# Kernel optimization log

Hardware: AMD Instinct MI355X
Metric: run time of the kernel (lower is better)

Reference implementation:

```python
import math
import jax, jax.numpy as jnp
import numpy as np

B, N, HID, NH = 4, 1024, 1024, 16
DH = HID // NH
MLP = int(HID * 4.0)


def _ndense(x, w):
    # NormalizedDense: row-normalize kernel (axis=1 for 2D), alpha=sqrt(w[0].size)=sqrt(out),
    # then divide by sqrt(fan_in).
    norm = jnp.linalg.norm(w, axis=1, keepdims=True)
    alpha = jnp.sqrt(jnp.asarray(w.shape[1], x.dtype))
    wn = w / (norm * alpha + 1e-4)
    wn = wn / jnp.sqrt(jnp.asarray(w.shape[0], x.dtype))
    return x @ wn


def mp_silu(x):
    return jax.nn.silu(x) / 0.596


def pixel_norm(x, eps=1e-4):
    return x * jax.lax.rsqrt(jnp.mean(x * x, axis=-1, keepdims=True) + eps)


def mp_add(a, b, t=0.3):
    return ((1 - t) * a + t * b) / math.sqrt((1 - t) ** 2 + t ** 2)


def setup_inputs() -> dict:
    key = jax.random.key(0)
    ks = jax.random.split(key, 9)
    std = 0.02
    return {
        "x": jax.random.normal(ks[0], (B, N, HID), jnp.float32),
        "c": jax.random.normal(ks[1], (B, HID), jnp.float32),
        "w_cond": std * jax.random.normal(ks[2], (HID, 2 * HID), jnp.float32),
        "w_qkv": std * jax.random.normal(ks[3], (HID, 3 * HID), jnp.float32),
        "w_out": std * jax.random.normal(ks[4], (HID, HID), jnp.float32),
        "w_mlp1": std * jax.random.normal(ks[5], (HID, MLP), jnp.float32),
        "w_mlp2": std * jax.random.normal(ks[6], (MLP, HID), jnp.float32),
        "attn_gain": 0.1 * jax.random.normal(ks[7], (), jnp.float32),
        "mlp_gain": 0.1 * jax.random.normal(ks[8], (), jnp.float32),
    }


def reference(x, c, w_cond, w_qkv, w_out, w_mlp1, w_mlp2, attn_gain, mlp_gain):
    # conditioning -> gain/shift
    cc = mp_silu(c)
    cc = _ndense(cc, w_cond)                       # [B, 2H]
    gain, shift = jnp.split(cc, 2, axis=-1)        # [B, H] each

    # attention branch
    x_cond = pixel_norm(x) * (1 + gain[:, None]) + shift[:, None]
    qkv = _ndense(x_cond, w_qkv)                   # [B, N, 3H]
    q, k, v = jnp.split(qkv, 3, axis=-1)
    q, k, v = pixel_norm(q), pixel_norm(k), pixel_norm(v)

    def split_heads(t):
        return t.reshape(B, N, NH, DH).transpose(0, 2, 1, 3)  # [B, NH, N, DH]

    q, k, v = split_heads(q), split_heads(k), split_heads(v)
    q = q / jnp.sqrt(jnp.sum(q * q, axis=-1, keepdims=True) + 1e-6)
    k = k / jnp.sqrt(jnp.sum(k * k, axis=-1, keepdims=True) + 1e-6)

    attn = jnp.einsum('bhnd,bhmd->bhnm', q, k) / math.sqrt(DH)
    attn = jax.nn.softmax(attn, axis=-1)
    x_attn = jnp.einsum('bhnm,bhmd->bhnd', attn, v)
    x_attn = x_attn.transpose(0, 2, 1, 3).reshape(B, N, HID)
    x_attn = pixel_norm(_ndense(x_attn, w_out)) * jnp.exp(attn_gain)
    x = mp_add(x, x_attn, t=0.3)

    # MLP branch
    x_cond = pixel_norm(x) * (1 + gain[:, None]) + shift[:, None]
    h = mp_silu(pixel_norm(_ndense(x_cond, w_mlp1)))
    x_mlp = pixel_norm(_ndense(h, w_mlp2)) * jnp.exp(mlp_gain)
    x = mp_add(x, x_mlp, t=0.3)
    return x
```

## Files before the change

kernel.cpp:

```cpp
#include <hip/hip_runtime.h>

typedef __bf16 bf16_t;
typedef __attribute__((ext_vector_type(8))) __bf16 bh8;
typedef __attribute__((ext_vector_type(4))) __bf16 bh4;
typedef __attribute__((ext_vector_type(4))) float f32x4;

#define DEV static __device__ __forceinline__

typedef __attribute__((address_space(3))) void lds_void;
typedef const __attribute__((address_space(1))) void glb_void;

DEV void async16(const bf16_t* g, bf16_t* l) {
  __builtin_amdgcn_global_load_lds((glb_void*)g, (lds_void*)l, 16, 0, 0);
}

#define GBAR() asm volatile("s_barrier" ::: "memory")
#define VMW(n) asm volatile("s_waitcnt vmcnt(" #n ")" ::: "memory")

DEV f32x4 mfma16(bh8 a, bh8 b, f32x4 c) {
  return __builtin_amdgcn_mfma_f32_16x16x32_bf16(a, b, c, 0, 0, 0);
}

DEV float wave_sum(float v) {
#pragma unroll
  for (int m = 32; m > 0; m >>= 1) v += __shfl_xor(v, m, 64);
  return v;
}

DEV float block_sum(float v, float* sbuf) {
  v = wave_sum(v);
  int wid = threadIdx.x >> 6;
  if ((threadIdx.x & 63) == 0) sbuf[wid] = v;
  __syncthreads();
  float r = sbuf[0] + sbuf[1] + sbuf[2] + sbuf[3];
  __syncthreads();
  return r;
}

__global__ void k_wnorm_all(const float* __restrict__ w_cond, const float* __restrict__ w_qkv,
                            const float* __restrict__ w_out, const float* __restrict__ w_mlp1,
                            const float* __restrict__ w_mlp2, float* __restrict__ s) {
  __shared__ float sbuf[4];
  int id = blockIdx.x;
  const float* W; int N, K, row;
  if (id < 1024)      { W = w_cond; N = 2048; K = 1024; row = id; }
  else if (id < 2048) { W = w_qkv;  N = 3072; K = 1024; row = id - 1024; }
  else if (id < 3072) { W = w_out;  N = 1024; K = 1024; row = id - 2048; }
  else if (id < 4096) { W = w_mlp1; N = 4096; K = 1024; row = id - 3072; }
  else                { W = w_mlp2; N = 1024; K = 4096; row = id - 4096; }
  const float4* wr = (const float4*)(W + (size_t)row * N);
  float acc = 0.f;
  for (int i = threadIdx.x; i < (N >> 2); i += 256) {
    float4 w = wr[i];
    acc += w.x*w.x + w.y*w.y + w.z*w.z + w.w*w.w;
  }
  float tot = block_sum(acc, sbuf);
  if (threadIdx.x == 0) {
    float norm = sqrtf(tot);
    s[id] = 1.0f / ((norm * sqrtf((float)N) + 1e-4f) * sqrtf((float)K));
  }
}

__global__ void k_wtrans_all(const float* __restrict__ w_cond, const float* __restrict__ w_qkv,
                             const float* __restrict__ w_out, const float* __restrict__ w_mlp1,
                             const float* __restrict__ w_mlp2, const float* __restrict__ sall,
                             bf16_t* __restrict__ wt_cond, bf16_t* __restrict__ wt_qkv,
                             bf16_t* __restrict__ wt_out, bf16_t* __restrict__ wt_mlp1,
                             bf16_t* __restrict__ wt_mlp2) {
  __shared__ float tile[64][65];
  int id = blockIdx.x;
  const float* W; const float* s; bf16_t* Wt; int K, N, n0, k0;
  if (id < 512)       { W=w_cond; s=sall;      Wt=wt_cond; K=1024; N=2048; int l=id;      n0=(l&31)*64; k0=(l>>5)*64; }
  else if (id < 1280) { W=w_qkv;  s=sall+1024; Wt=wt_qkv;  K=1024; N=3072; int l=id-512;  n0=(l%48)*64; k0=(l/48)*64; }
  else if (id < 1536) { W=w_out;  s=sall+2048; Wt=wt_out;  K=1024; N=1024; int l=id-1280; n0=(l&15)*64; k0=(l>>4)*64; }
  else if (id < 2560) { W=w_mlp1; s=sall+3072; Wt=wt_mlp1; K=1024; N=4096; int l=id-1536; n0=(l&63)*64; k0=(l>>6)*64; }
  else                { W=w_mlp2; s=sall+4096; Wt=wt_mlp2; K=4096; N=1024; int l=id-2560; n0=(l&15)*64; k0=(l>>4)*64; }
  int tx = threadIdx.x & 63, ty = threadIdx.x >> 6;
  for (int r = ty; r < 64; r += 4)
    tile[r][tx] = W[(size_t)(k0 + r) * N + n0 + tx] * s[k0 + r];
  __syncthreads();
  for (int r = ty; r < 64; r += 4)
    Wt[(size_t)(n0 + r) * K + k0 + tx] = (bf16_t)tile[tx][r];
}

__global__ void k_cond(const float* __restrict__ c, const bf16_t* __restrict__ wt,
                       float* __restrict__ gs) {
  __shared__ float cc[4][1024];
  int t = threadIdx.x;
  for (int i = t; i < 4096; i += 256) {
    int b = i >> 10, col = i & 1023;
    float x = c[b * 1024 + col];
    float sig = 1.f / (1.f + __expf(-x));
    cc[b][col] = x * sig * (1.f / 0.596f);
  }
  __syncthreads();
  int wid = t >> 6, lane = t & 63;
  int j = blockIdx.x * 4 + wid;
  const bf16_t* wr = wt + (size_t)j * 1024;
  float acc0 = 0, acc1 = 0, acc2 = 0, acc3 = 0;
  for (int i = lane; i < 1024; i += 64) {
    float w = (float)wr[i];
    acc0 += cc[0][i] * w; acc1 += cc[1][i] * w;
    acc2 += cc[2][i] * w; acc3 += cc[3][i] * w;
  }
  float v0 = wave_sum(acc0), v1 = wave_sum(acc1), v2 = wave_sum(acc2), v3 = wave_sum(acc3);
  if (lane == 0) {
    gs[0 * 2048 + j] = v0; gs[1 * 2048 + j] = v1;
    gs[2 * 2048 + j] = v2; gs[3 * 2048 + j] = v3;
  }
}

__global__ void k_xcond(const float* __restrict__ x, const float* __restrict__ gs,
                        bf16_t* __restrict__ xc) {
  __shared__ float sbuf[4];
  int row = blockIdx.x, b = row >> 10, t = threadIdx.x;
  float4 v = ((const float4*)(x + (size_t)row * 1024))[t];
  float ss = v.x*v.x + v.y*v.y + v.z*v.z + v.w*v.w;
  float tot = block_sum(ss, sbuf);
  float r = rsqrtf(tot * (1.f/1024.f) + 1e-4f);
  float4 g  = ((const float4*)(gs + b * 2048))[t];
  float4 sh = ((const float4*)(gs + b * 2048 + 1024))[t];
  bh4 o;
  o[0] = (bf16_t)(v.x * r * (1.f + g.x) + sh.x);
  o[1] = (bf16_t)(v.y * r * (1.f + g.y) + sh.y);
  o[2] = (bf16_t)(v.z * r * (1.f + g.z) + sh.z);
  o[3] = (bf16_t)(v.w * r * (1.f + g.w) + sh.w);
  *(bh4*)(xc + (size_t)row * 1024 + t * 4) = o;
}

__global__ __launch_bounds__(512, 2) void k_gemm8(const bf16_t* __restrict__ A,
                                                  const bf16_t* __restrict__ Bt,
                                                  bf16_t* __restrict__ C,
                                                  int M, int N, int K, int klen) {
  __shared__ __attribute__((aligned(16))) bf16_t As[2][2][256][32];
  __shared__ __attribute__((aligned(16))) bf16_t Bs[2][2][256][32];
  const int ntn = gridDim.x;
  const unsigned flat = blockIdx.x + ntn * blockIdx.y;
  const unsigned q = (ntn * gridDim.y) >> 3;
  const unsigned wg = (flat & 7) * q + (flat >> 3);
  const int m0 = (int)(wg / (unsigned)ntn) * 256;
  const int n0 = (int)(wg % (unsigned)ntn) * 256;
  const size_t kbeg = (size_t)blockIdx.z * klen;
  C += (size_t)blockIdx.z * M * N;
  const int t = threadIdx.x, lane = t & 63;
  const int wm = (t >> 6) >> 2, wn = (t >> 6) & 3;
  const int l15 = lane & 15, quad = lane >> 4;
  const int q8 = (quad ^ ((l15 >> 2) & 2)) * 8;
  const int rA = wm * 128 + l15;
  const int rB = wn * 64 + l15;
  const int sr = t >> 2;
  const int sc = ((t & 3) << 3) ^ ((t & 32) >> 1);
  const int swv = (t >> 6) * 512;
  const bf16_t* AgS = A + (size_t)(m0 + sr) * K + kbeg + sc;
  const bf16_t* BgS = Bt + (size_t)(n0 + sr) * K + kbeg + sc;
  const size_t rstep = (size_t)128 * K;
  const int NT = klen >> 6;
  f32x4 acc[8][4] = {};

#define STG_A(kt_, h_, bb_) { const bf16_t* g = AgS + (kt_) * 64 + (h_) * 32; \
    bf16_t* l = &As[bb_][h_][0][0] + swv; async16(g, l); async16(g + rstep, l + 4096); }
#define STG_B(kt_, h_, bb_) { const bf16_t* g = BgS + (kt_) * 64 + (h_) * 32; \
    bf16_t* l = &Bs[bb_][h_][0][0] + swv; async16(g, l); async16(g + rstep, l + 4096); }

  STG_B(0, 0, 0); STG_B(0, 1, 0);
  STG_A(0, 0, 0); STG_A(0, 1, 0);
  if (NT > 1) { STG_B(1, 0, 1); STG_B(1, 1, 1); VMW(4); } else { VMW(0); }
  GBAR();

  for (int kt = 0; kt < NT; ++kt) {
    const int bb = kt & 1;
    bh8 a[4][2], b[4][2];
#pragma unroll
    for (int m = 0; m < 4; ++m)
#pragma unroll
      for (int kc = 0; kc < 2; ++kc)
        a[m][kc] = *(const bh8*)&As[bb][kc][rA + m * 16][q8];
#pragma unroll
    for (int n = 0; n < 2; ++n)
#pragma unroll
      for (int kc = 0; kc < 2; ++kc)
        b[n][kc] = *(const bh8*)&Bs[bb][kc][rB + n * 16][q8];
    if (kt + 1 < NT) STG_A(kt + 1, 0, bb ^ 1);
    GBAR();
    __builtin_amdgcn_s_setprio(1);
#pragma unroll
    for (int m = 0; m < 4; ++m)
#pragma unroll
      for (int n = 0; n < 2; ++n)
#pragma unroll
        for (int kc = 0; kc < 2; ++kc)
          acc[m][n] = mfma16(a[m][kc], b[n][kc], acc[m][n]);
    __builtin_amdgcn_s_setprio(0);
    GBAR();
#pragma unroll
    for (int n = 0; n < 2; ++n)
#pragma unroll
      for (int kc = 0; kc < 2; ++kc)
        b[2 + n][kc] = *(const bh8*)&Bs[bb][kc][rB + (2 + n) * 16][q8];
    if (kt + 1 < NT) STG_A(kt + 1, 1, bb ^ 1);
    GBAR();
    __builtin_amdgcn_s_setprio(1);
#pragma unroll
    for (int m = 0; m < 4; ++m)
#pragma unroll
      for (int n = 0; n < 2; ++n)
#pragma unroll
        for (int kc = 0; kc < 2; ++kc)
          acc[m][2 + n] = mfma16(a[m][kc], b[2 + n][kc], acc[m][2 + n]);
    __builtin_amdgcn_s_setprio(0);
    GBAR();
#pragma unroll
    for (int m = 0; m < 4; ++m)
#pragma unroll
      for (int kc = 0; kc < 2; ++kc)
        a[m][kc] = *(const bh8*)&As[bb][kc][rA + 64 + m * 16][q8];
    if (kt + 2 < NT) STG_B(kt + 2, 0, bb);
    GBAR();
    __builtin_amdgcn_s_setprio(1);
#pragma unroll
    for (int m = 0; m < 4; ++m)
#pragma unroll
      for (int n = 0; n < 2; ++n)
#pragma unroll
        for (int kc = 0; kc < 2; ++kc)
          acc[4 + m][n] = mfma16(a[m][kc], b[n][kc], acc[4 + m][n]);
    __builtin_amdgcn_s_setprio(0);
    GBAR();
    if (kt + 2 < NT) STG_B(kt + 2, 1, bb);
    __builtin_amdgcn_s_setprio(1);
#pragma unroll
    for (int m = 0; m < 4; ++m)
#pragma unroll
      for (int n = 0; n < 2; ++n)
#pragma unroll
        for (int kc = 0; kc < 2; ++kc)
          acc[4 + m][2 + n] = mfma16(a[m][kc], b[2 + n][kc], acc[4 + m][2 + n]);
    __builtin_amdgcn_s_setprio(0);
    if (kt + 2 < NT) { VMW(4); } else { VMW(0); }
    GBAR();
  }
#undef STG_A
#undef STG_B

  const int cm = m0 + wm * 128 + quad * 4;
  const int cn = n0 + wn * 64 + l15;
#pragma unroll
  for (int m = 0; m < 8; ++m)
#pragma unroll
    for (int n = 0; n < 4; ++n)
#pragma unroll
      for (int r2 = 0; r2 < 4; ++r2)
        C[(size_t)(cm + m * 16 + r2) * N + cn + n * 16] = (bf16_t)acc[m][n][r2];
}

__global__ void k_qkvnorm(const bf16_t* __restrict__ qkv, bf16_t* __restrict__ qo,
                          bf16_t* __restrict__ ko, bf16_t* __restrict__ vo) {
  __shared__ float sbuf[4];
  const int row = blockIdx.x, b = row >> 10, n = row & 1023, t = threadIdx.x;
  const bf16_t* rp = qkv + (size_t)row * 3072;
  bh4 q4 = *(const bh4*)(rp + t * 4);
  bh4 k4 = *(const bh4*)(rp + 1024 + t * 4);
  bh4 v4 = *(const bh4*)(rp + 2048 + t * 4);
  float4 q = {(float)q4[0], (float)q4[1], (float)q4[2], (float)q4[3]};
  float4 k = {(float)k4[0], (float)k4[1], (float)k4[2], (float)k4[3]};
  float4 v = {(float)v4[0], (float)v4[1], (float)v4[2], (float)v4[3]};
  float sq = q.x*q.x + q.y*q.y + q.z*q.z + q.w*q.w;
  float sk = k.x*k.x + k.y*k.y + k.z*k.z + k.w*k.w;
  float sv = v.x*v.x + v.y*v.y + v.z*v.z + v.w*v.w;
  float tq = block_sum(sq, sbuf);
  float tk = block_sum(sk, sbuf);
  float tv = block_sum(sv, sbuf);
  float rq = rsqrtf(tq * (1.f/1024.f) + 1e-4f);
  float rk = rsqrtf(tk * (1.f/1024.f) + 1e-4f);
  float rv = rsqrtf(tv * (1.f/1024.f) + 1e-4f);
  float hq = sq, hk = sk;
#pragma unroll
  for (int m = 1; m < 16; m <<= 1) { hq += __shfl_xor(hq, m, 64); hk += __shfl_xor(hk, m, 64); }
  float qs = rq * rsqrtf(rq*rq*hq + 1e-6f);
  float ks = rk * rsqrtf(rk*rk*hk + 1e-6f);
  int h = t >> 4, d = (t & 15) * 4;
  size_t base = ((size_t)(b * 16 + h) * 1024 + n) * 64 + d;
  bh4 oq, okk, ov;
  oq[0]=(bf16_t)(q.x*qs); oq[1]=(bf16_t)(q.y*qs); oq[2]=(bf16_t)(q.z*qs); oq[3]=(bf16_t)(q.w*qs);
  okk[0]=(bf16_t)(k.x*ks); okk[1]=(bf16_t)(k.y*ks); okk[2]=(bf16_t)(k.z*ks); okk[3]=(bf16_t)(k.w*ks);
  ov[0]=(bf16_t)(v.x*rv); ov[1]=(bf16_t)(v.y*rv); ov[2]=(bf16_t)(v.z*rv); ov[3]=(bf16_t)(v.w*rv);
  *(bh4*)(qo + base) = oq;
  *(bh4*)(ko + base) = okk;
  *(bh4*)(vo + base) = ov;
}

__global__ void k_vtrans(const bf16_t* __restrict__ vh, bf16_t* __restrict__ vt) {
  __shared__ bf16_t tile[64][72];
  const int n0 = blockIdx.x * 64, bh = blockIdx.y;
  const int t = threadIdx.x;
  const bf16_t* src = vh + ((size_t)bh * 1024 + n0) * 64;
#pragma unroll
  for (int i = t; i < 512; i += 256) {
    int r = i >> 3, p = (i & 7) * 8;
    *(bh8*)&tile[r][p] = *(const bh8*)(src + r * 64 + p);
  }
  __syncthreads();
  bf16_t* dst = vt + (size_t)bh * 64 * 1024 + n0;
#pragma unroll
  for (int i = t; i < 512; i += 256) {
    int d = i & 63, nch = (i >> 6) * 8;
    bh8 o;
#pragma unroll
    for (int j = 0; j < 8; j++) o[j] = tile[nch + j][d];
    *(bh8*)(dst + (size_t)d * 1024 + nch) = o;
  }
}

__global__ __launch_bounds__(256) void k_attn(const bf16_t* __restrict__ Q,
                                              const bf16_t* __restrict__ K,
                                              const bf16_t* __restrict__ Vt_g,
                                              bf16_t* __restrict__ O) {
  __shared__ bf16_t Qs[64][72];
  __shared__ bf16_t Ks[64][72];
  __shared__ bf16_t Vt[64][72];
  __shared__ bf16_t Ps[64][72];
  const int qt = blockIdx.x, bh = blockIdx.y;
  const int b = bh >> 4, h = bh & 15;
  const int t = threadIdx.x, lane = t & 63, wid = t >> 6;
  const int l15 = lane & 15, quad = lane >> 4;
  const int strip = wid * 16;
  const bf16_t* Qg = Q + ((size_t)bh * 1024 + qt * 64) * 64;
  const bf16_t* Kg = K + (size_t)bh * 1024 * 64;
  const bf16_t* Vg = Vt_g + (size_t)bh * 64 * 1024;
  for (int i = t; i < 512; i += 256) {
    int r = i >> 3, p = (i & 7) * 8;
    *(bh8*)&Qs[r][p] = *(const bh8*)(Qg + r * 64 + p);
  }
  f32x4 o[4] = {};
  float rs[4] = {};
  __syncthreads();
  for (int kv0 = 0; kv0 < 1024; kv0 += 64) {
    for (int i = t; i < 512; i += 256) {
      int r = i >> 3, p = (i & 7) * 8;
      *(bh8*)&Ks[r][p] = *(const bh8*)(Kg + (size_t)(kv0 + r) * 64 + p);
      *(bh8*)&Vt[r][p] = *(const bh8*)(Vg + (size_t)r * 1024 + kv0 + p);
    }
    __syncthreads();
    f32x4 s[4] = {};
#pragma unroll
    for (int kc = 0; kc < 2; kc++) {
      bh8 aq = *(const bh8*)&Qs[strip + l15][kc*32 + quad*8];
      bh8 bk[4];
#pragma unroll
      for (int j = 0; j < 4; j++) bk[j] = *(const bh8*)&Ks[j*16 + l15][kc*32 + quad*8];
#pragma unroll
      for (int j = 0; j < 4; j++)
        s[j] = __builtin_amdgcn_mfma_f32_16x16x32_bf16(aq, bk[j], s[j], 0, 0, 0);
    }
#pragma unroll
    for (int j = 0; j < 4; j++)
#pragma unroll
      for (int r = 0; r < 4; r++) {
        float p = __expf(s[j][r] * 0.125f);
        bf16_t pb = (bf16_t)p;
        rs[r] += (float)pb;
        Ps[strip + quad*4 + r][j*16 + l15] = pb;
      }
#pragma unroll
    for (int kc = 0; kc < 2; kc++) {
      bh8 ap = *(const bh8*)&Ps[strip + l15][kc*32 + quad*8];
      bh8 bv[4];
#pragma unroll
      for (int j = 0; j < 4; j++) bv[j] = *(const bh8*)&Vt[j*16 + l15][kc*32 + quad*8];
#pragma unroll
      for (int j = 0; j < 4; j++)
        o[j] = __builtin_amdgcn_mfma_f32_16x16x32_bf16(ap, bv[j], o[j], 0, 0, 0);
    }
    __syncthreads();
  }
#pragma unroll
  for (int r = 0; r < 4; r++) {
    float v = rs[r];
    v += __shfl_xor(v, 1, 64); v += __shfl_xor(v, 2, 64);
    v += __shfl_xor(v, 4, 64); v += __shfl_xor(v, 8, 64);
    float inv = 1.f / v;
    int n = qt * 64 + strip + quad*4 + r;
#pragma unroll
    for (int j = 0; j < 4; j++)
      O[((size_t)b * 1024 + n) * 1024 + h*64 + j*16 + l15] = (bf16_t)(o[j][r] * inv);
  }
}

__global__ void k_amerge(const bf16_t* __restrict__ y, const float* __restrict__ x,
                         const float* __restrict__ gs, const float* __restrict__ again,
                         bf16_t* __restrict__ x1, bf16_t* __restrict__ xc2) {
  __shared__ float sbuf[4];
  int row = blockIdx.x, b = row >> 10, t = threadIdx.x;
  const size_t PS = (size_t)4096 * 1024;
  float4 yv = {0.f, 0.f, 0.f, 0.f};
#pragma unroll
  for (int p = 0; p < 4; p++) {
    bh4 a = *(const bh4*)(y + p * PS + (size_t)row * 1024 + t * 4);
    yv.x += (float)a[0]; yv.y += (float)a[1]; yv.z += (float)a[2]; yv.w += (float)a[3];
  }
  float4 xv = ((const float4*)(x + (size_t)row * 1024))[t];
  float ss = yv.x*yv.x + yv.y*yv.y + yv.z*yv.z + yv.w*yv.w;
  float tot = block_sum(ss, sbuf);
  float r = rsqrtf(tot * (1.f/1024.f) + 1e-4f);
  float ag = __expf(again[0]);
  const float C1 = 0.7f / 0.76157731059f, C2 = 0.3f / 0.76157731059f;
  float4 xo;
  xo.x = C1 * xv.x + C2 * (yv.x * r * ag);
  xo.y = C1 * xv.y + C2 * (yv.y * r * ag);
  xo.z = C1 * xv.z + C2 * (yv.z * r * ag);
  xo.w = C1 * xv.w + C2 * (yv.w * r * ag);
  bh4 x1o;
  x1o[0] = (bf16_t)xo.x; x1o[1] = (bf16_t)xo.y; x1o[2] = (bf16_t)xo.z; x1o[3] = (bf16_t)xo.w;
  *(bh4*)(x1 + (size_t)row * 1024 + t * 4) = x1o;
  float ss1 = xo.x*xo.x + xo.y*xo.y + xo.z*xo.z + xo.w*xo.w;
  float tot1 = block_sum(ss1, sbuf);
  float r1 = rsqrtf(tot1 * (1.f/1024.f) + 1e-4f);
  float4 g  = ((const float4*)(gs + b * 2048))[t];
  float4 sh = ((const float4*)(gs + b * 2048 + 1024))[t];
  bh4 o;
  o[0] = (bf16_t)(xo.x * r1 * (1.f + g.x) + sh.x);
  o[1] = (bf16_t)(xo.y * r1 * (1.f + g.y) + sh.y);
  o[2] = (bf16_t)(xo.z * r1 * (1.f + g.z) + sh.z);
  o[3] = (bf16_t)(xo.w * r1 * (1.f + g.w) + sh.w);
  *(bh4*)(xc2 + (size_t)row * 1024 + t * 4) = o;
}

__global__ void k_mlpnorm(const bf16_t* __restrict__ hf, bf16_t* __restrict__ hb) {
  __shared__ float sbuf[4];
  int row = blockIdx.x, t = threadIdx.x;
  const bf16_t* rp = hf + (size_t)row * 4096;
  float4 v[4]; float ss = 0.f;
#pragma unroll
  for (int i = 0; i < 4; i++) {
    bh4 bv = *(const bh4*)(rp + (t + 256 * i) * 4);
    v[i].x = (float)bv[0]; v[i].y = (float)bv[1]; v[i].z = (float)bv[2]; v[i].w = (float)bv[3];
    ss += v[i].x*v[i].x + v[i].y*v[i].y + v[i].z*v[i].z + v[i].w*v[i].w;
  }
  float tot = block_sum(ss, sbuf);
  float r = rsqrtf(tot * (1.f/4096.f) + 1e-4f);
#pragma unroll
  for (int i = 0; i < 4; i++) {
    float a[4] = {v[i].x, v[i].y, v[i].z, v[i].w};
    bh4 o;
#pragma unroll
    for (int j = 0; j < 4; j++) {
      float u = a[j] * r;
      float sig = 1.f / (1.f + __expf(-u));
      o[j] = (bf16_t)(u * sig * (1.f / 0.596f));
    }
    *(bh4*)(hb + (size_t)row * 4096 + (t + 256 * i) * 4) = o;
  }
}

__global__ void k_fmerge(const bf16_t* __restrict__ y, const bf16_t* __restrict__ x1,
                         const float* __restrict__ mgain, float* __restrict__ out) {
  __shared__ float sbuf[4];
  int row = blockIdx.x, t = threadIdx.x;
  const size_t PS = (size_t)4096 * 1024;
  float4 yv = {0.f, 0.f, 0.f, 0.f};
#pragma unroll
  for (int p = 0; p < 4; p++) {
    bh4 yp = *(const bh4*)(y + p * PS + (size_t)row * 1024 + t * 4);
    yv.x += (float)yp[0]; yv.y += (float)yp[1]; yv.z += (float)yp[2]; yv.w += (float)yp[3];
  }
  bh4 xb = *(const bh4*)(x1 + (size_t)row * 1024 + t * 4);
  float4 xv = {(float)xb[0], (float)xb[1], (float)xb[2], (float)xb[3]};
  float ss = yv.x*yv.x + yv.y*yv.y + yv.z*yv.z + yv.w*yv.w;
  float tot = block_sum(ss, sbuf);
  float r = rsqrtf(tot * (1.f/1024.f) + 1e-4f);
  float mg = __expf(mgain[0]);
  const float C1 = 0.7f / 0.76157731059f, C2 = 0.3f / 0.76157731059f;
  float4 o;
  o.x = C1 * xv.x + C2 * (yv.x * r * mg);
  o.y = C1 * xv.y + C2 * (yv.y * r * mg);
  o.z = C1 * xv.z + C2 * (yv.z * r * mg);
  o.w = C1 * xv.w + C2 * (yv.w * r * mg);
  ((float4*)(out + (size_t)row * 1024))[t] = o;
}

extern "C" void kernel_launch(void* const* d_in, const int* in_sizes, int n_in,
                              void* d_out, int out_size, void* d_ws, size_t ws_size,
                              hipStream_t stream) {
  const float* x      = (const float*)d_in[0];
  const float* c      = (const float*)d_in[1];
  const float* w_cond = (const float*)d_in[2];
  const float* w_qkv  = (const float*)d_in[3];
  const float* w_out  = (const float*)d_in[4];
  const float* w_mlp1 = (const float*)d_in[5];
  const float* w_mlp2 = (const float*)d_in[6];
  const float* again  = (const float*)d_in[7];
  const float* mgain  = (const float*)d_in[8];
  float* out = (float*)d_out;
  char* ws = (char*)d_ws;

  bf16_t* wt_cond = (bf16_t*)(ws + 0);
  bf16_t* wt_qkv  = (bf16_t*)(ws + 4194304);
  bf16_t* wt_out  = (bf16_t*)(ws + 10485760);
  bf16_t* wt_mlp1 = (bf16_t*)(ws + 12582912);
  bf16_t* wt_mlp2 = (bf16_t*)(ws + 20971520);
  float*  sn      = (float*)(ws + 29360128);
  float*  gs      = (float*)(ws + 29392896);
  bf16_t* xc      = (bf16_t*)(ws + 29425664);
  bf16_t* qh      = (bf16_t*)(ws + 37814272);
  bf16_t* kh      = (bf16_t*)(ws + 46202880);
  bf16_t* vh      = (bf16_t*)(ws + 54591488);
  bf16_t* xattn   = (bf16_t*)(ws + 62980096);
  bf16_t* hb      = (bf16_t*)(ws + 37814272);
  bf16_t* x1      = (bf16_t*)(ws + 71368704);
  bf16_t* vt      = (bf16_t*)(ws + 79757312);
  bf16_t* buf_b   = (bf16_t*)(ws + 88145920);

  k_wnorm_all<<<8192, 256, 0, stream>>>(w_cond, w_qkv, w_out, w_mlp1, w_mlp2, sn);
  k_wtrans_all<<<3584, 256, 0, stream>>>(w_cond, w_qkv, w_out, w_mlp1, w_mlp2, sn,
                                         wt_cond, wt_qkv, wt_out, wt_mlp1, wt_mlp2);

  k_cond<<<512, 256, 0, stream>>>(c, wt_cond, gs);
  k_xcond<<<4096, 256, 0, stream>>>(x, gs, xc);
  k_gemm8<<<dim3(12, 16, 1), 512, 0, stream>>>(xc, wt_qkv, buf_b, 4096, 3072, 1024, 1024);
  k_qkvnorm<<<4096, 256, 0, stream>>>(buf_b, qh, kh, vh);
  k_vtrans<<<dim3(16, 64), 256, 0, stream>>>(vh, vt);
  k_attn<<<dim3(16, 64), 256, 0, stream>>>(qh, kh, vt, xattn);
  k_gemm8<<<dim3(4, 16, 4), 512, 0, stream>>>(xattn, wt_out, buf_b, 4096, 1024, 1024, 256);
  k_amerge<<<4096, 256, 0, stream>>>(buf_b, x, gs, again, x1, xc);
  k_gemm8<<<dim3(16, 16, 1), 512, 0, stream>>>(xc, wt_mlp1, buf_b, 4096, 4096, 1024, 1024);
  k_mlpnorm<<<4096, 256, 0, stream>>>(buf_b, hb);
  k_gemm8<<<dim3(4, 16, 4), 512, 0, stream>>>(hb, wt_mlp2, buf_b, 4096, 1024, 4096, 1024);
  k_fmerge<<<4096, 256, 0, stream>>>(buf_b, x1, mgain, out);
  (void)in_sizes; (void)n_in; (void)out_size; (void)ws_size;
}
```

Baseline: 368.9 us.

## Restructure attention kernel with async double-buffered K/V, swizzled LDS, 128-row Q tiles

Rewrites the attention kernel so each block handles 128 query rows (two 16-row fragments per wave) and streams K/V tiles with async global-to-LDS loads into double buffers, overlapping the next tile's load with the current tile's compute. LDS tiles drop their padding and use XOR swizzling to avoid bank conflicts. Grid blocks are remapped so neighbouring blocks share heads, and MFMA sections are wrapped in s_setprio. The aim is to hide memory latency and reuse each K/V tile across twice as many queries. The cost is more registers per thread and fewer blocks in the grid.

```diff
diff --git a/kernel.cpp b/kernel.cpp
--- a/kernel.cpp
+++ b/kernel.cpp
@@ -19,6 +19,14 @@
 
 DEV f32x4 mfma16(bh8 a, bh8 b, f32x4 c) {
   return __builtin_amdgcn_mfma_f32_16x16x32_bf16(a, b, c, 0, 0, 0);
+}
+
+DEV const bf16_t* lds7(const bf16_t* base, int row, int c) {
+  return base + row * 64 + ((c ^ (row & 7)) << 3);
+}
+DEV bf16_t* ldsP(bf16_t* base, int row, int c) {
+  int m = (row & 7) ^ ((row >> 3) & 1);
+  return base + row * 64 + ((c ^ m) << 3);
 }
 
 DEV float wave_sum(float v) {
@@ -311,79 +319,121 @@
   }
 }
 
-__global__ __launch_bounds__(256) void k_attn(const bf16_t* __restrict__ Q,
-                                              const bf16_t* __restrict__ K,
-                                              const bf16_t* __restrict__ Vt_g,
-                                              bf16_t* __restrict__ O) {
-  __shared__ bf16_t Qs[64][72];
-  __shared__ bf16_t Ks[64][72];
-  __shared__ bf16_t Vt[64][72];
-  __shared__ bf16_t Ps[64][72];
-  const int qt = blockIdx.x, bh = blockIdx.y;
+__global__ __launch_bounds__(256, 2) void k_attn(const bf16_t* __restrict__ Q,
+                                                 const bf16_t* __restrict__ K,
+                                                 const bf16_t* __restrict__ Vt_g,
+                                                 bf16_t* __restrict__ O) {
+  __shared__ __attribute__((aligned(16))) bf16_t Qs[128][64];
+  __shared__ __attribute__((aligned(16))) bf16_t Ks[2][64][64];
+  __shared__ __attribute__((aligned(16))) bf16_t Vt[2][64][64];
+  __shared__ __attribute__((aligned(16))) bf16_t Ps[128][64];
+  const unsigned flat = blockIdx.x + 8u * blockIdx.y;
+  const int qt = (int)((flat >> 3) & 7);
+  const int bh = (int)((flat & 7) * 8 + (flat >> 6));
   const int b = bh >> 4, h = bh & 15;
   const int t = threadIdx.x, lane = t & 63, wid = t >> 6;
   const int l15 = lane & 15, quad = lane >> 4;
-  const int strip = wid * 16;
-  const bf16_t* Qg = Q + ((size_t)bh * 1024 + qt * 64) * 64;
+  const int strip = wid * 32;
+  const int srow = t >> 3;
+  const int scol = ((t & 7) ^ (srow & 7)) << 3;
+  const int swv = wid * 512;
+  const bf16_t* Qg = Q + ((size_t)bh * 1024 + qt * 128) * 64;
   const bf16_t* Kg = K + (size_t)bh * 1024 * 64;
   const bf16_t* Vg = Vt_g + (size_t)bh * 64 * 1024;
-  for (int i = t; i < 512; i += 256) {
-    int r = i >> 3, p = (i & 7) * 8;
-    *(bh8*)&Qs[r][p] = *(const bh8*)(Qg + r * 64 + p);
-  }
-  f32x4 o[4] = {};
-  float rs[4] = {};
-  __syncthreads();
-  for (int kv0 = 0; kv0 < 1024; kv0 += 64) {
-    for (int i = t; i < 512; i += 256) {
-      int r = i >> 3, p = (i & 7) * 8;
-      *(bh8*)&Ks[r][p] = *(const bh8*)(Kg + (size_t)(kv0 + r) * 64 + p);
-      *(bh8*)&Vt[r][p] = *(const bh8*)(Vg + (size_t)r * 1024 + kv0 + p);
+
+#pragma unroll
+  for (int c2 = 0; c2 < 4; ++c2)
+    async16(Qg + (size_t)(c2 * 32 + srow) * 64 + scol, &Qs[0][0] + c2 * 2048 + swv);
+#pragma unroll
+  for (int r0 = 0; r0 < 64; r0 += 32) {
+    async16(Kg + (size_t)(r0 + srow) * 64 + scol, &Ks[0][0][0] + r0 * 64 + swv);
+    async16(Vg + (size_t)(r0 + srow) * 1024 + scol, &Vt[0][0][0] + r0 * 64 + swv);
+  }
+  VMW(0);
+  GBAR();
+
+  f32x4 o[2][4] = {};
+  float rs[2][4] = {{}, {}};
+  for (int kt = 0; kt < 16; ++kt) {
+    const int bb = kt & 1;
+    const int kv0 = kt * 64;
+    if (kt < 15) {
+#pragma unroll
+      for (int r0 = 0; r0 < 64; r0 += 32) {
+        async16(Kg + (size_t)(kv0 + 64 + r0 + srow) * 64 + scol,
+                &Ks[bb ^ 1][0][0] + r0 * 64 + swv);
+        async16(Vg + (size_t)(r0 + srow) * 1024 + kv0 + 64 + scol,
+                &Vt[bb ^ 1][0][0] + r0 * 64 + swv);
+      }
     }
-    __syncthreads();
-    f32x4 s[4] = {};
-#pragma unroll
-    for (int kc = 0; kc < 2; kc++) {
-      bh8 aq = *(const bh8*)&Qs[strip + l15][kc*32 + quad*8];
-      bh8 bk[4];
-#pragma unroll
-      for (int j = 0; j < 4; j++) bk[j] = *(const bh8*)&Ks[j*16 + l15][kc*32 + quad*8];
-#pragma unroll
-      for (int j = 0; j < 4; j++)
-        s[j] = __builtin_amdgcn_mfma_f32_16x16x32_bf16(aq, bk[j], s[j], 0, 0, 0);
+    f32x4 s[2][4] = {};
+    bh8 aq[2][2], bk[4][2];
+#pragma unroll
+    for (int rf = 0; rf < 2; ++rf)
+#pragma unroll
+      for (int kc = 0; kc < 2; ++kc)
+        aq[rf][kc] = *(const bh8*)lds7(&Qs[0][0], strip + rf * 16 + l15, kc * 4 + quad);
+#pragma unroll
+    for (int j = 0; j < 4; ++j)
+#pragma unroll
+      for (int kc = 0; kc < 2; ++kc)
+        bk[j][kc] = *(const bh8*)lds7(&Ks[bb][0][0], j * 16 + l15, kc * 4 + quad);
+    __builtin_amdgcn_s_setprio(1);
+#pragma unroll
+    for (int rf = 0; rf < 2; ++rf)
+#pragma unroll
+      for (int j = 0; j < 4; ++j)
+#pragma unroll
+        for (int kc = 0; kc < 2; ++kc)
+          s[rf][j] = mfma16(aq[rf][kc], bk[j][kc], s[rf][j]);
+    __builtin_amdgcn_s_setprio(0);
+#pragma unroll
+    for (int rf = 0; rf < 2; ++rf)
+#pragma unroll
+      for (int j = 0; j < 4; ++j)
+#pragma unroll
+        for (int r = 0; r < 4; ++r) {
+          float p = __expf(s[rf][j][r] * 0.125f);
+          bf16_t pb = (bf16_t)p;
+          rs[rf][r] += (float)pb;
+          int prow = strip + rf * 16 + quad * 4 + r;
+          ldsP(&Ps[0][0], prow, j * 2 + (l15 >> 3))[l15 & 7] = pb;
+        }
+    bh8 ap[2][2], bv[4][2];
+#pragma unroll
+    for (int rf = 0; rf < 2; ++rf)
+#pragma unroll
+      for (int kc = 0; kc < 2; ++kc)
+        ap[rf][kc] = *(const bh8*)ldsP(&Ps[0][0], strip + rf * 16 + l15, kc * 4 + quad);
+#pragma unroll
+    for (int j = 0; j < 4; ++j)
+#pragma unroll
+      for (int kc = 0; kc < 2; ++kc)
+        bv[j][kc] = *(const bh8*)lds7(&Vt[bb][0][0], j * 16 + l15, kc * 4 + quad);
+    __builtin_amdgcn_s_setprio(1);
+#pragma unroll
+    for (int rf = 0; rf < 2; ++rf)
+#pragma unroll
+      for (int j = 0; j < 4; ++j)
+#pragma unroll
+        for (int kc = 0; kc < 2; ++kc)
+          o[rf][j] = mfma16(ap[rf][kc], bv[j][kc], o[rf][j]);
+    __builtin_amdgcn_s_setprio(0);
+    if (kt < 15) { VMW(0); GBAR(); }
+  }
+#pragma unroll
+  for (int rf = 0; rf < 2; ++rf)
+#pragma unroll
+    for (int r = 0; r < 4; ++r) {
+      float v = rs[rf][r];
+      v += __shfl_xor(v, 1, 64); v += __shfl_xor(v, 2, 64);
+      v += __shfl_xor(v, 4, 64); v += __shfl_xor(v, 8, 64);
+      float inv = 1.f / v;
+      int n = qt * 128 + strip + rf * 16 + quad * 4 + r;
+#pragma unroll
+      for (int j = 0; j < 4; ++j)
+        O[((size_t)b * 1024 + n) * 1024 + h * 64 + j * 16 + l15] = (bf16_t)(o[rf][j][r] * inv);
     }
-#pragma unroll
-    for (int j = 0; j < 4; j++)
-#pragma unroll
-      for (int r = 0; r < 4; r++) {
-        float p = __expf(s[j][r] * 0.125f);
-        bf16_t pb = (bf16_t)p;
-        rs[r] += (float)pb;
-        Ps[strip + quad*4 + r][j*16 + l15] = pb;
-      }
-#pragma unroll
-    for (int kc = 0; kc < 2; kc++) {
-      bh8 ap = *(const bh8*)&Ps[strip + l15][kc*32 + quad*8];
-      bh8 bv[4];
-#pragma unroll
-      for (int j = 0; j < 4; j++) bv[j] = *(const bh8*)&Vt[j*16 + l15][kc*32 + quad*8];
-#pragma unroll
-      for (int j = 0; j < 4; j++)
-        o[j] = __builtin_amdgcn_mfma_f32_16x16x32_bf16(ap, bv[j], o[j], 0, 0, 0);
-    }
-    __syncthreads();
-  }
-#pragma unroll
-  for (int r = 0; r < 4; r++) {
-    float v = rs[r];
-    v += __shfl_xor(v, 1, 64); v += __shfl_xor(v, 2, 64);
-    v += __shfl_xor(v, 4, 64); v += __shfl_xor(v, 8, 64);
-    float inv = 1.f / v;
-    int n = qt * 64 + strip + quad*4 + r;
-#pragma unroll
-    for (int j = 0; j < 4; j++)
-      O[((size_t)b * 1024 + n) * 1024 + h*64 + j*16 + l15] = (bf16_t)(o[j][r] * inv);
-  }
 }
 
 __global__ void k_amerge(const bf16_t* __restrict__ y, const float* __restrict__ x,
@@ -519,7 +569,7 @@
   k_gemm8<<<dim3(12, 16, 1), 512, 0, stream>>>(xc, wt_qkv, buf_b, 4096, 3072, 1024, 1024);
   k_qkvnorm<<<4096, 256, 0, stream>>>(buf_b, qh, kh, vh);
   k_vtrans<<<dim3(16, 64), 256, 0, stream>>>(vh, vt);
-  k_attn<<<dim3(16, 64), 256, 0, stream>>>(qh, kh, vt, xattn);
+  k_attn<<<dim3(8, 64), 256, 0, stream>>>(qh, kh, vt, xattn);
   k_gemm8<<<dim3(4, 16, 4), 512, 0, stream>>>(xattn, wt_out, buf_b, 4096, 1024, 1024, 256);
   k_amerge<<<4096, 256, 0, stream>>>(buf_b, x, gs, again, x1, xc);
   k_gemm8<<<dim3(16, 16, 1), 512, 0, stream>>>(xc, wt_mlp1, buf_b, 4096, 4096, 1024, 1024);
```

Result: faster. 357.2 us (-3.2%).
